# Kernel optimization log

Hardware: AMD Instinct MI355X
Metric: run time of the kernel (lower is better)

## Reference

```python
import jax, jax.numpy as jnp
import numpy as np

N, D, DEG, DEPTH, H = 50000, 300, 6, 3, 4
E = N * DEG
DK = D // H


def setup_inputs() -> dict:
    key = jax.random.key(0)
    ks = jax.random.split(key, 14)
    # circulant molecular-like graph: node i <-> i+k (k=1,2,3), edges emitted in
    # reverse pairs (2t, 2t+1) as required by reverse_edge()
    u = np.arange(N)
    src_l, dst_l = [], []
    for k in (1, 2, 3):
        v = (u + k) % N
        src_l.append(np.stack([u, v], 1).reshape(-1))
        dst_l.append(np.stack([v, u], 1).reshape(-1))
    src = np.concatenate(src_l).astype(np.int32)
    dst = np.concatenate(dst_l).astype(np.int32)
    # incoming-edge ids per node (every node has exactly DEG in-edges)
    order = np.argsort(dst, kind='stable')
    nbr_eids = order.reshape(N, DEG).astype(np.int32)
    nbr_mask = np.ones((N, DEG), dtype=bool)
    sd = 1.0 / np.sqrt(D)
    p = lambda i, shape: jax.random.normal(ks[i], shape, jnp.float32) * sd
    return {
        'f': jax.random.normal(ks[0], (N, D), jnp.float32),
        'x': jax.random.normal(ks[1], (E, D), jnp.float32),
        'Wq': p(2, (D, D)), 'bq': jnp.zeros((D,), jnp.float32),
        'Wk': p(3, (D, D)), 'bk': jnp.zeros((D,), jnp.float32),
        'Wv': p(4, (D, D)), 'bv': jnp.zeros((D,), jnp.float32),
        'Wo': p(5, (D, D)), 'bo': jnp.zeros((D,), jnp.float32),
        'W_mp': p(6, (DEPTH - 1, D, D)), 'b_mp': jnp.zeros((DEPTH - 1, D), jnp.float32),
        'W_last': p(7, (3 * D, D)), 'b_last': jnp.zeros((D,), jnp.float32),
        'src': jnp.asarray(src), 'dst': jnp.asarray(dst),
        'nbr_eids': jnp.asarray(nbr_eids), 'nbr_mask': jnp.asarray(nbr_mask),
    }


def reference(f, x, Wq, bq, Wk, bk, Wv, bv, Wo, bo, W_mp, b_mp, W_last, b_last,
              src, dst, nbr_eids, nbr_mask):
    n = f.shape[0]
    e = x.shape[0]
    rev = jnp.arange(e) ^ 1                     # reverse-pair permutation
    has_in = nbr_mask.any(axis=-1)              # [N]
    scale = 1.0 / jnp.sqrt(jnp.float32(DK))
    h = x                                       # edge state 'h' init from 'x'
    f_h = f                                     # node state 'f_h' init from 'f'
    for i in range(DEPTH - 1):
        # ragged mailbox of incoming edge states, padded to DEG
        m = jnp.where(nbr_mask[..., None], h[nbr_eids], 0.0)        # [N,DEG,D]
        q = (f_h @ Wq + bq).reshape(n, H, DK)                        # query = node feat
        k = (m @ Wk + bk).reshape(n, DEG, H, DK)                     # key   = mailbox
        v = ((m + f_h[:, None, :]) @ Wv + bv).reshape(n, DEG, H, DK) # value = mailbox + feat
        scores = jnp.einsum('nhk,ndhk->nhd', q, k) * scale          # [N,H,DEG]
        scores = jnp.where(nbr_mask[:, None, :], scores, -1e9)
        attn = jax.nn.softmax(scores, axis=-1)
        out = jnp.einsum('nhd,ndhk->nhk', attn, v).reshape(n, D) @ Wo + bo
        f_h = jnp.where(has_in[:, None], out, f_h)
        # edge update: m = f_h[src] - rev_h; h = relu(x + Linear_i(m))
        m_e = f_h[src] - h[rev]
        h = jax.nn.relu(x + m_e @ W_mp[i] + b_mp[i])
    # GEANet is undefined in the provided source -> identity pass-through
    mail = jax.ops.segment_sum(h, dst, num_segments=n)              # sum of in-edge states
    f_new = jnp.concatenate([mail, f_h, f], axis=-1) @ W_last + b_last
    f_final = jnp.where(has_in[:, None], f_new, f_h)
    return f_final, h
```

## Files before the change

kernel.cpp:

```cpp
#include <hip/hip_runtime.h>
#include <hip/hip_bf16.h>

typedef unsigned long long ull;
typedef unsigned int u32;
typedef unsigned short u16;
typedef __hip_bfloat16 bf16;
typedef __attribute__((ext_vector_type(8))) short v8s;
typedef __attribute__((ext_vector_type(4))) float v4f;
typedef __attribute__((ext_vector_type(2))) ull v2u;

#define NN 50000
#define DD 300
#define PD 320
#define EE (NN*6)

__device__ __forceinline__ u16 f2bf(float f) {
    u32 u = __float_as_uint(f);
    u32 r = u + 0x7FFFu + ((u >> 16) & 1u);
    return (u16)(r >> 16);
}
__device__ __forceinline__ float bf2f(u16 b) { return __uint_as_float(((u32)b) << 16); }

__device__ __forceinline__ ull sub4bf(ull a, ull b) {
    ull r = 0;
    #pragma unroll
    for (int i = 0; i < 4; ++i) {
        float fa = bf2f((u16)(a >> (16 * i)));
        float fb = bf2f((u16)(b >> (16 * i)));
        r |= ((ull)f2bf(fa - fb)) << (16 * i);
    }
    return r;
}

enum { A_DIR = 0, A_MPG = 1, A_CAT = 2 };
enum { E_BIAS = 0, E_RELUX = 1 };
enum { O_F32 = 1, O_BF16 = 2, O_BOTH = 3 };

template<int AMODE, int EPI, int OUTM, int NW, int NSEG>
__global__ __launch_bounds__(NW*64)
void gemm_mfma(const bf16* __restrict__ A0, const bf16* __restrict__ A1,
               const bf16* __restrict__ A2, const int* __restrict__ srcidx,
               const bf16* __restrict__ BT,
               const float* __restrict__ bias0, const float* __restrict__ bias1,
               const bf16* __restrict__ xepi,
               float* __restrict__ Cf, bf16* __restrict__ Cb0, bf16* __restrict__ Cb1,
               int M)
{
    __shared__ __align__(16) char Als[64 * 640];
    const int tid = threadIdx.x;
    const int wave = tid >> 6, lane = tid & 63;
    const int l15 = lane & 15, l4 = lane >> 4;
    const int wv = (NW == 8) ? (wave & 3) : wave;
    const int half = (NW == 8) ? (wave >> 2) : 0;
    const int rowBase = blockIdx.x * 64;
    const int T = NW * 64;

    v4f acc[4][5];
    const v4f vzero = {0.f, 0.f, 0.f, 0.f};
    #pragma unroll
    for (int mt = 0; mt < 4; ++mt)
        #pragma unroll
        for (int nt = 0; nt < 5; ++nt) acc[mt][nt] = vzero;

    for (int seg = 0; seg < NSEG; ++seg) {
        const bf16* As = (seg == 0) ? A0 : (seg == 1 ? A1 : A2);
        if (seg) __syncthreads();
        #pragma unroll
        for (int s = 0; s < 2560 / T; ++s) {
            int c = tid + T * s;
            int r = c / 40, ch = c - r * 40;
            int grow = rowBase + r;
            int gc = (grow < M) ? grow : 0;
            v2u v;
            if (AMODE == A_MPG) {
                int s0 = srcidx[gc];
                v2u a = *(const v2u*)(A0 + (long)s0 * PD + ch * 8);
                v2u b = *(const v2u*)(A1 + (long)(gc ^ 1) * PD + ch * 8);
                v[0] = sub4bf(a[0], b[0]);
                v[1] = sub4bf(a[1], b[1]);
            } else {
                v = *(const v2u*)(As + (long)gc * PD + ch * 8);
            }
            *(v2u*)(Als + ((c * 16) ^ ((r & 7) << 4))) = v;
        }
        __syncthreads();

        const bf16* BTs = BT + (long)seg * 320 * PD;
        #pragma unroll
        for (int ks = 0; ks < 10; ++ks) {
            v8s af[4];
            #pragma unroll
            for (int mt = 0; mt < 4; ++mt) {
                int rowL = mt * 16 + l15;
                af[mt] = *(const v8s*)(Als +
                    ((rowL * 640 + ks * 64 + l4 * 16) ^ ((rowL & 7) << 4)));
            }
            #pragma unroll
            for (int nt = 0; nt < 5; ++nt) {
                int col = wave * 80 + nt * 16 + l15;
                v8s bfr = *(const v8s*)(BTs + (long)col * PD + ks * 32 + l4 * 8);
                #pragma unroll
                for (int mt = 0; mt < 4; ++mt)
                    acc[mt][nt] = __builtin_amdgcn_mfma_f32_16x16x32_bf16(
                        af[mt], bfr, acc[mt][nt], 0, 0, 0);
            }
        }
        if (seg + 1 < NSEG) __syncthreads();
    }

    const int NOUT = (NW == 8) ? 2 : 1;
    #pragma unroll
    for (int oh = 0; oh < NOUT; ++oh) {
        __syncthreads();
        if (half == oh) {
            const float* bias = oh ? bias1 : bias0;
            #pragma unroll
            for (int nt = 0; nt < 5; ++nt) {
                int col = wv * 80 + nt * 16 + l15;
                float bvv = (bias && col < DD) ? bias[col] : 0.f;
                #pragma unroll
                for (int mt = 0; mt < 4; ++mt) {
                    #pragma unroll
                    for (int r = 0; r < 4; ++r) {
                        int rowL = mt * 16 + l4 * 4 + r;
                        int grow = rowBase + rowL;
                        float v = acc[mt][nt][r] + bvv;
                        if (EPI == E_RELUX) {
                            v += bf2f(((const u16*)xepi)[(long)grow * PD + col]);
                            v = fmaxf(v, 0.f);
                        }
                        if (col >= DD) v = 0.f;
                        if ((OUTM & O_F32) && grow < M && col < DD)
                            Cf[(long)grow * DD + col] = v;
                        if (OUTM & O_BF16) {
                            int addr = (rowL * 640 + col * 2) ^ (((rowL >> 2) & 7) << 4);
                            *(u16*)(Als + addr) = f2bf(v);
                        }
                    }
                }
            }
        }
        if (OUTM & O_BF16) {
            __syncthreads();
            bf16* Cb = oh ? Cb1 : Cb0;
            #pragma unroll
            for (int s = 0; s < 2560 / T; ++s) {
                int c = tid + T * s;
                int r = c / 40;
                int grow = rowBase + r;
                if (grow < M)
                    *(v2u*)(Cb + (long)grow * PD + (c - r * 40) * 8) =
                        *(const v2u*)(Als + ((c * 16) ^ (((r >> 2) & 7) << 4)));
            }
        }
    }
}

__global__ __launch_bounds__(256)
void attn_k(const bf16* __restrict__ Q, const bf16* __restrict__ FV,
            const bf16* __restrict__ Kk, const bf16* __restrict__ HV,
            const int* __restrict__ nbr, bf16* __restrict__ out)
{
    int wave = threadIdx.x >> 6, lane = threadIdx.x & 63;
    int n = blockIdx.x * 4 + wave;
    if (n >= NN) return;
    int eid[6];
    #pragma unroll
    for (int d = 0; d < 6; ++d) eid[d] = nbr[n * 6 + d];

    bool act = lane < 40;
    int cl = act ? lane : 0;
    long qo = (long)n * PD + cl * 8;
    v2u qv = *(const v2u*)(Q + qo);
    v2u fvv = *(const v2u*)(FV + qo);
    float qf[8], fvf[8];
    int hx[8];
    #pragma unroll
    for (int i = 0; i < 8; ++i) {
        u16 qr = (u16)(qv[i >> 2] >> ((i & 3) * 16));
        u16 fr = (u16)(fvv[i >> 2] >> ((i & 3) * 16));
        qf[i] = act ? bf2f(qr) : 0.f;
        fvf[i] = act ? bf2f(fr) : 0.f;
        int h = (cl * 8 + i) / 75;
        hx[i] = h > 3 ? 3 : h;
    }

    float s0[6], s1[6], s2[6], s3[6];
    #pragma unroll
    for (int d = 0; d < 6; ++d) {
        v2u kv = *(const v2u*)(Kk + (long)eid[d] * PD + cl * 8);
        float p0 = 0, p1 = 0, p2 = 0, p3 = 0;
        #pragma unroll
        for (int i = 0; i < 8; ++i) {
            float kf = bf2f((u16)(kv[i >> 2] >> ((i & 3) * 16)));
            float pr = qf[i] * kf;
            p0 += (hx[i] == 0) ? pr : 0.f;
            p1 += (hx[i] == 1) ? pr : 0.f;
            p2 += (hx[i] == 2) ? pr : 0.f;
            p3 += (hx[i] == 3) ? pr : 0.f;
        }
        #pragma unroll
        for (int off = 32; off; off >>= 1) {
            p0 += __shfl_xor(p0, off);
            p1 += __shfl_xor(p1, off);
            p2 += __shfl_xor(p2, off);
            p3 += __shfl_xor(p3, off);
        }
        s0[d] = p0; s1[d] = p1; s2[d] = p2; s3[d] = p3;
    }

    const float scale = 0.1154700538379252f;
    float at0[6], at1[6], at2[6], at3[6];
    {
        float m0 = -1e30f, m1 = -1e30f, m2 = -1e30f, m3 = -1e30f;
        #pragma unroll
        for (int d = 0; d < 6; ++d) {
            s0[d] *= scale; s1[d] *= scale; s2[d] *= scale; s3[d] *= scale;
            m0 = fmaxf(m0, s0[d]); m1 = fmaxf(m1, s1[d]);
            m2 = fmaxf(m2, s2[d]); m3 = fmaxf(m3, s3[d]);
        }
        float t0 = 0, t1 = 0, t2 = 0, t3 = 0;
        #pragma unroll
        for (int d = 0; d < 6; ++d) {
            at0[d] = expf(s0[d] - m0); t0 += at0[d];
            at1[d] = expf(s1[d] - m1); t1 += at1[d];
            at2[d] = expf(s2[d] - m2); t2 += at2[d];
            at3[d] = expf(s3[d] - m3); t3 += at3[d];
        }
        t0 = 1.f / t0; t1 = 1.f / t1; t2 = 1.f / t2; t3 = 1.f / t3;
        #pragma unroll
        for (int d = 0; d < 6; ++d) {
            at0[d] *= t0; at1[d] *= t1; at2[d] *= t2; at3[d] *= t3;
        }
    }

    float o[8];
    #pragma unroll
    for (int i = 0; i < 8; ++i) o[i] = fvf[i];
    #pragma unroll
    for (int d = 0; d < 6; ++d) {
        v2u hv = *(const v2u*)(HV + (long)eid[d] * PD + cl * 8);
        #pragma unroll
        for (int i = 0; i < 8; ++i) {
            float a = at0[d];
            a = (hx[i] == 1) ? at1[d] : a;
            a = (hx[i] == 2) ? at2[d] : a;
            a = (hx[i] == 3) ? at3[d] : a;
            o[i] += a * bf2f((u16)(hv[i >> 2] >> ((i & 3) * 16)));
        }
    }
    if (act) {
        v2u r;
        r[0] = (ull)f2bf(o[0]) | ((ull)f2bf(o[1]) << 16) |
               ((ull)f2bf(o[2]) << 32) | ((ull)f2bf(o[3]) << 48);
        r[1] = (ull)f2bf(o[4]) | ((ull)f2bf(o[5]) << 16) |
               ((ull)f2bf(o[6]) << 32) | ((ull)f2bf(o[7]) << 48);
        *(v2u*)(out + qo) = r;
    }
}

__global__ __launch_bounds__(256)
void mail_k(const bf16* __restrict__ h, const int* __restrict__ nbr,
            bf16* __restrict__ mail)
{
    int idx = blockIdx.x * 256 + threadIdx.x;
    if (idx >= NN * 40) return;
    int n = idx / 40, ch = idx - n * 40;
    const int* e = nbr + n * 6;
    float s[8] = {0, 0, 0, 0, 0, 0, 0, 0};
    #pragma unroll
    for (int d = 0; d < 6; ++d) {
        v2u v = *(const v2u*)(h + (long)e[d] * PD + ch * 8);
        #pragma unroll
        for (int i = 0; i < 8; ++i)
            s[i] += bf2f((u16)(v[i >> 2] >> ((i & 3) * 16)));
    }
    v2u r;
    r[0] = (ull)f2bf(s[0]) | ((ull)f2bf(s[1]) << 16) |
           ((ull)f2bf(s[2]) << 32) | ((ull)f2bf(s[3]) << 48);
    r[1] = (ull)f2bf(s[4]) | ((ull)f2bf(s[5]) << 16) |
           ((ull)f2bf(s[6]) << 32) | ((ull)f2bf(s[7]) << 48);
    *(v2u*)(mail + (long)n * PD + ch * 8) = r;
}

__global__ __launch_bounds__(256)
void conv_k(const float* __restrict__ in, bf16* __restrict__ out, int rows)
{
    long idx = (long)blockIdx.x * 256 + threadIdx.x;
    if (idx >= (long)rows * 40) return;
    int r = (int)(idx / 40), ch = (int)(idx - (long)r * 40);
    int c4 = ch * 2;
    float4 a = {0, 0, 0, 0}, b = {0, 0, 0, 0};
    if (c4 < 75)     a = *(const float4*)(in + (long)r * DD + c4 * 4);
    if (c4 + 1 < 75) b = *(const float4*)(in + (long)r * DD + c4 * 4 + 4);
    v2u v;
    v[0] = (ull)f2bf(a.x) | ((ull)f2bf(a.y) << 16) |
           ((ull)f2bf(a.z) << 32) | ((ull)f2bf(a.w) << 48);
    v[1] = (ull)f2bf(b.x) | ((ull)f2bf(b.y) << 16) |
           ((ull)f2bf(b.z) << 32) | ((ull)f2bf(b.w) << 48);
    *(v2u*)(out + (long)r * PD + ch * 8) = v;
}

__global__ __launch_bounds__(256)
void tw_k(const float* __restrict__ W, bf16* __restrict__ BT)
{
    int idx = blockIdx.x * 256 + threadIdx.x;
    if (idx >= 320 * 320) return;
    int nn = idx / 320, kk = idx - nn * 320;
    u16 v = 0;
    if (nn < DD && kk < DD) v = f2bf(W[kk * DD + nn]);
    ((u16*)BT)[idx] = v;
}

extern "C" void kernel_launch(void* const* d_in, const int* in_sizes, int n_in,
                              void* d_out, int out_size, void* d_ws, size_t ws_size,
                              hipStream_t stream)
{
    const float* f     = (const float*)d_in[0];
    const float* x     = (const float*)d_in[1];
    const float* Wq    = (const float*)d_in[2];
    const float* bq    = (const float*)d_in[3];
    const float* Wk    = (const float*)d_in[4];
    const float* bk    = (const float*)d_in[5];
    const float* Wv    = (const float*)d_in[6];
    const float* bv    = (const float*)d_in[7];
    const float* Wo    = (const float*)d_in[8];
    const float* bo    = (const float*)d_in[9];
    const float* Wmp   = (const float*)d_in[10];
    const float* bmp   = (const float*)d_in[11];
    const float* Wlast = (const float*)d_in[12];
    const float* blast = (const float*)d_in[13];
    const int*   src   = (const int*)d_in[14];
    const int*   nbr   = (const int*)d_in[16];

    float* out     = (float*)d_out;
    float* f_final = out;
    float* h_final = out + (long)NN * DD;

    char* ws = (char*)d_ws;
    bf16* xb  = (bf16*)(ws);
    bf16* h1b = (bf16*)(ws + 192000000LL);
    bf16* Kkb = (bf16*)(ws + 384000000LL);
    bf16* HVb = (bf16*)(ws + 576000000LL);
    bf16* fb  = (bf16*)(ws + 768000000LL);
    bf16* Qb  = (bf16*)(ws + 800000000LL);
    bf16* FVb = (bf16*)(ws + 832000000LL);
    bf16* FHb = (bf16*)(ws + 864000000LL);
    bf16* BT0 = (bf16*)(ws + 896000000LL);
    bf16* AOb = Qb;
    bf16* MLb = Qb;
    auto btp = [&](int i) { return BT0 + (long)i * 320 * 320; };

    dim3 blk(256), blk8(512);
    const int gE = (EE + 63) / 64;
    const int gN = (NN + 63) / 64;

    conv_k<<<(int)(((long)EE * 40 + 255) / 256), blk, 0, stream>>>(x, xb, EE);
    conv_k<<<(int)(((long)NN * 40 + 255) / 256), blk, 0, stream>>>(f, fb, NN);
    tw_k<<<400, blk, 0, stream>>>(Wq, btp(0));
    tw_k<<<400, blk, 0, stream>>>(Wv, btp(1));
    tw_k<<<400, blk, 0, stream>>>(Wk, btp(2));
    tw_k<<<400, blk, 0, stream>>>(Wv, btp(3));
    tw_k<<<400, blk, 0, stream>>>(Wo, btp(4));
    tw_k<<<400, blk, 0, stream>>>(Wmp, btp(5));
    tw_k<<<400, blk, 0, stream>>>(Wmp + 90000, btp(6));
    tw_k<<<400, blk, 0, stream>>>(Wlast, btp(7));
    tw_k<<<400, blk, 0, stream>>>(Wlast + 90000, btp(8));
    tw_k<<<400, blk, 0, stream>>>(Wlast + 180000, btp(9));

    for (int it = 0; it < 2; ++it) {
        const bf16* hb  = it ? h1b : xb;
        const bf16* fhb = it ? FHb : fb;
        gemm_mfma<A_DIR, E_BIAS, O_BF16, 8, 1><<<gE, blk8, 0, stream>>>(
            hb, nullptr, nullptr, nullptr, btp(2), bk, bv, nullptr,
            nullptr, Kkb, HVb, EE);
        gemm_mfma<A_DIR, E_BIAS, O_BF16, 8, 1><<<gN, blk8, 0, stream>>>(
            fhb, nullptr, nullptr, nullptr, btp(0), bq, nullptr, nullptr,
            nullptr, Qb, FVb, NN);
        attn_k<<<(NN + 3) / 4, blk, 0, stream>>>(Qb, FVb, Kkb, HVb, nbr, AOb);
        gemm_mfma<A_DIR, E_BIAS, O_BF16, 4, 1><<<gN, blk, 0, stream>>>(
            AOb, nullptr, nullptr, nullptr, btp(4), bo, nullptr, nullptr,
            nullptr, FHb, nullptr, NN);
        if (it == 0) {
            gemm_mfma<A_MPG, E_RELUX, O_BF16, 4, 1><<<gE, blk, 0, stream>>>(
                FHb, hb, nullptr, src, btp(5), bmp, nullptr, xb,
                nullptr, h1b, nullptr, EE);
        } else {
            gemm_mfma<A_MPG, E_RELUX, O_BOTH, 4, 1><<<gE, blk, 0, stream>>>(
                FHb, hb, nullptr, src, btp(6), bmp + DD, nullptr, xb,
                h_final, HVb, nullptr, EE);
        }
    }

    mail_k<<<(NN * 40 + 255) / 256, blk, 0, stream>>>(HVb, nbr, MLb);
    gemm_mfma<A_CAT, E_BIAS, O_F32, 4, 3><<<gN, blk, 0, stream>>>(
        MLb, FHb, fb, nullptr, btp(7), blast, nullptr, nullptr,
        f_final, nullptr, nullptr, NN);
}
```

Measured before the change: 2.438 ms.

## Fold Wq·Wkᵀ and Wv·Wo per head to drop edge-sized K/V GEMMs

Reassociates the attention maths so keys and values are never projected per edge. Per-head query-key matrices (Wq_h·Wk_hᵀ) and value-output matrices (Wv_h·Wo_h) are precomputed once. Scores then become dot products of node-side G_h against the raw incoming edge states, and attention-weighted sums of raw edge states feed a five-segment node GEMM. This removes the large E×D K/V GEMM from each iteration, at the cost of more node-side GEMM work, bf16-rounded composed weights, and a GEMM epilogue that now rounds to bf16 before the residual add and fp32 output.

```diff
diff --git a/kernel.cpp b/kernel.cpp
--- a/kernel.cpp
+++ b/kernel.cpp
@@ -39,8 +39,9 @@
 template<int AMODE, int EPI, int OUTM, int NW, int NSEG>
 __global__ __launch_bounds__(NW*64)
 void gemm_mfma(const bf16* __restrict__ A0, const bf16* __restrict__ A1,
-               const bf16* __restrict__ A2, const int* __restrict__ srcidx,
-               const bf16* __restrict__ BT,
+               const bf16* __restrict__ A2, const bf16* __restrict__ A3,
+               const bf16* __restrict__ A4,
+               const int* __restrict__ srcidx, const bf16* __restrict__ BT,
                const float* __restrict__ bias0, const float* __restrict__ bias1,
                const bf16* __restrict__ xepi,
                float* __restrict__ Cf, bf16* __restrict__ Cb0, bf16* __restrict__ Cb1,
@@ -63,7 +64,8 @@
         for (int nt = 0; nt < 5; ++nt) acc[mt][nt] = vzero;
 
     for (int seg = 0; seg < NSEG; ++seg) {
-        const bf16* As = (seg == 0) ? A0 : (seg == 1 ? A1 : A2);
+        const bf16* As = (seg == 0) ? A0 : (seg == 1 ? A1 : (seg == 2 ? A2 :
+                         (seg == 3 ? A3 : A4)));
         if (seg) __syncthreads();
         #pragma unroll
         for (int s = 0; s < 2560 / T; ++s) {
@@ -117,49 +119,75 @@
             #pragma unroll
             for (int nt = 0; nt < 5; ++nt) {
                 int col = wv * 80 + nt * 16 + l15;
-                float bvv = (bias && col < DD) ? bias[col] : 0.f;
+                float bvv = bias ? bias[col] : 0.f;
                 #pragma unroll
                 for (int mt = 0; mt < 4; ++mt) {
                     #pragma unroll
                     for (int r = 0; r < 4; ++r) {
                         int rowL = mt * 16 + l4 * 4 + r;
-                        int grow = rowBase + rowL;
-                        float v = acc[mt][nt][r] + bvv;
-                        if (EPI == E_RELUX) {
-                            v += bf2f(((const u16*)xepi)[(long)grow * PD + col]);
-                            v = fmaxf(v, 0.f);
+                        *(u16*)(Als + ((rowL * 640 + col * 2) ^ (((rowL >> 2) & 7) << 4)))
+                            = f2bf(acc[mt][nt][r] + bvv);
+                    }
+                }
+            }
+        }
+        __syncthreads();
+        {
+            bf16* Cb = oh ? Cb1 : Cb0;
+            #pragma unroll
+            for (int s = 0; s < 2560 / T; ++s) {
+                int c = tid + T * s;
+                int r = c / 40, ch = c - r * 40;
+                int grow = rowBase + r;
+                if (grow >= M) continue;
+                v2u val = *(const v2u*)(Als + ((c * 16) ^ (((r >> 2) & 7) << 4)));
+                if (EPI == E_RELUX) {
+                    v2u xv = *(const v2u*)(xepi + (long)grow * PD + ch * 8);
+                    #pragma unroll
+                    for (int w = 0; w < 2; ++w) {
+                        ull rr = 0;
+                        #pragma unroll
+                        for (int i = 0; i < 4; ++i) {
+                            float fv = bf2f((u16)(val[w] >> (16 * i))) +
+                                       bf2f((u16)(xv[w] >> (16 * i)));
+                            fv = fmaxf(fv, 0.f);
+                            rr |= ((ull)f2bf(fv)) << (16 * i);
                         }
-                        if (col >= DD) v = 0.f;
-                        if ((OUTM & O_F32) && grow < M && col < DD)
-                            Cf[(long)grow * DD + col] = v;
-                        if (OUTM & O_BF16) {
-                            int addr = (rowL * 640 + col * 2) ^ (((rowL >> 2) & 7) << 4);
-                            *(u16*)(Als + addr) = f2bf(v);
+                        val[w] = rr;
+                    }
+                }
+                if (OUTM & O_BF16)
+                    *(v2u*)(Cb + (long)grow * PD + ch * 8) = val;
+                if (OUTM & O_F32) {
+                    int col0 = ch * 8;
+                    if (col0 < DD) {
+                        float4 lo;
+                        lo.x = bf2f((u16)(val[0]));
+                        lo.y = bf2f((u16)(val[0] >> 16));
+                        lo.z = bf2f((u16)(val[0] >> 32));
+                        lo.w = bf2f((u16)(val[0] >> 48));
+                        *(float4*)(Cf + (long)grow * DD + col0) = lo;
+                        if (col0 + 4 < DD) {
+                            float4 hi;
+                            hi.x = bf2f((u16)(val[1]));
+                            hi.y = bf2f((u16)(val[1] >> 16));
+                            hi.z = bf2f((u16)(val[1] >> 32));
+                            hi.w = bf2f((u16)(val[1] >> 48));
+                            *(float4*)(Cf + (long)grow * DD + col0 + 4) = hi;
                         }
                     }
                 }
             }
         }
-        if (OUTM & O_BF16) {
-            __syncthreads();
-            bf16* Cb = oh ? Cb1 : Cb0;
-            #pragma unroll
-            for (int s = 0; s < 2560 / T; ++s) {
-                int c = tid + T * s;
-                int r = c / 40;
-                int grow = rowBase + r;
-                if (grow < M)
-                    *(v2u*)(Cb + (long)grow * PD + (c - r * 40) * 8) =
-                        *(const v2u*)(Als + ((c * 16) ^ (((r >> 2) & 7) << 4)));
-            }
-        }
-    }
-}
-
-__global__ __launch_bounds__(256)
-void attn_k(const bf16* __restrict__ Q, const bf16* __restrict__ FV,
-            const bf16* __restrict__ Kk, const bf16* __restrict__ HV,
-            const int* __restrict__ nbr, bf16* __restrict__ out)
+    }
+}
+
+__global__ __launch_bounds__(256)
+void scoreU_k(const bf16* __restrict__ G0, const bf16* __restrict__ G1,
+              const bf16* __restrict__ G2, const bf16* __restrict__ G3,
+              const bf16* __restrict__ h, const int* __restrict__ nbr,
+              bf16* __restrict__ U0, bf16* __restrict__ U1,
+              bf16* __restrict__ U2, bf16* __restrict__ U3)
 {
     int wave = threadIdx.x >> 6, lane = threadIdx.x & 63;
     int n = blockIdx.x * 4 + wave;
@@ -170,34 +198,33 @@
 
     bool act = lane < 40;
     int cl = act ? lane : 0;
-    long qo = (long)n * PD + cl * 8;
-    v2u qv = *(const v2u*)(Q + qo);
-    v2u fvv = *(const v2u*)(FV + qo);
-    float qf[8], fvf[8];
-    int hx[8];
-    #pragma unroll
-    for (int i = 0; i < 8; ++i) {
-        u16 qr = (u16)(qv[i >> 2] >> ((i & 3) * 16));
-        u16 fr = (u16)(fvv[i >> 2] >> ((i & 3) * 16));
-        qf[i] = act ? bf2f(qr) : 0.f;
-        fvf[i] = act ? bf2f(fr) : 0.f;
-        int h = (cl * 8 + i) / 75;
-        hx[i] = h > 3 ? 3 : h;
-    }
+    long go = (long)n * PD + cl * 8;
+
+    float g[4][8];
+    #pragma unroll
+    for (int hh = 0; hh < 4; ++hh) {
+        const bf16* Gp = (hh == 0) ? G0 : (hh == 1) ? G1 : (hh == 2) ? G2 : G3;
+        v2u gv = *(const v2u*)(Gp + go);
+        #pragma unroll
+        for (int i = 0; i < 8; ++i)
+            g[hh][i] = act ? bf2f((u16)(gv[i >> 2] >> ((i & 3) * 16))) : 0.f;
+    }
+    v2u hp[6];
+    #pragma unroll
+    for (int d = 0; d < 6; ++d)
+        hp[d] = *(const v2u*)(h + (long)eid[d] * PD + cl * 8);
 
     float s0[6], s1[6], s2[6], s3[6];
     #pragma unroll
     for (int d = 0; d < 6; ++d) {
-        v2u kv = *(const v2u*)(Kk + (long)eid[d] * PD + cl * 8);
         float p0 = 0, p1 = 0, p2 = 0, p3 = 0;
         #pragma unroll
         for (int i = 0; i < 8; ++i) {
-            float kf = bf2f((u16)(kv[i >> 2] >> ((i & 3) * 16)));
-            float pr = qf[i] * kf;
-            p0 += (hx[i] == 0) ? pr : 0.f;
-            p1 += (hx[i] == 1) ? pr : 0.f;
-            p2 += (hx[i] == 2) ? pr : 0.f;
-            p3 += (hx[i] == 3) ? pr : 0.f;
+            float hf = bf2f((u16)(hp[d][i >> 2] >> ((i & 3) * 16)));
+            p0 += g[0][i] * hf;
+            p1 += g[1][i] * hf;
+            p2 += g[2][i] * hf;
+            p3 += g[3][i] * hf;
         }
         #pragma unroll
         for (int off = 32; off; off >>= 1) {
@@ -210,7 +237,7 @@
     }
 
     const float scale = 0.1154700538379252f;
-    float at0[6], at1[6], at2[6], at3[6];
+    float at[4][6];
     {
         float m0 = -1e30f, m1 = -1e30f, m2 = -1e30f, m3 = -1e30f;
         #pragma unroll
@@ -222,40 +249,45 @@
         float t0 = 0, t1 = 0, t2 = 0, t3 = 0;
         #pragma unroll
         for (int d = 0; d < 6; ++d) {
-            at0[d] = expf(s0[d] - m0); t0 += at0[d];
-            at1[d] = expf(s1[d] - m1); t1 += at1[d];
-            at2[d] = expf(s2[d] - m2); t2 += at2[d];
-            at3[d] = expf(s3[d] - m3); t3 += at3[d];
+            at[0][d] = expf(s0[d] - m0); t0 += at[0][d];
+            at[1][d] = expf(s1[d] - m1); t1 += at[1][d];
+            at[2][d] = expf(s2[d] - m2); t2 += at[2][d];
+            at[3][d] = expf(s3[d] - m3); t3 += at[3][d];
         }
         t0 = 1.f / t0; t1 = 1.f / t1; t2 = 1.f / t2; t3 = 1.f / t3;
         #pragma unroll
         for (int d = 0; d < 6; ++d) {
-            at0[d] *= t0; at1[d] *= t1; at2[d] *= t2; at3[d] *= t3;
-        }
-    }
-
-    float o[8];
-    #pragma unroll
-    for (int i = 0; i < 8; ++i) o[i] = fvf[i];
+            at[0][d] *= t0; at[1][d] *= t1; at[2][d] *= t2; at[3][d] *= t3;
+        }
+    }
+
+    float u[4][8];
+    #pragma unroll
+    for (int hh = 0; hh < 4; ++hh)
+        #pragma unroll
+        for (int i = 0; i < 8; ++i) u[hh][i] = 0.f;
     #pragma unroll
     for (int d = 0; d < 6; ++d) {
-        v2u hv = *(const v2u*)(HV + (long)eid[d] * PD + cl * 8);
         #pragma unroll
         for (int i = 0; i < 8; ++i) {
-            float a = at0[d];
-            a = (hx[i] == 1) ? at1[d] : a;
-            a = (hx[i] == 2) ? at2[d] : a;
-            a = (hx[i] == 3) ? at3[d] : a;
-            o[i] += a * bf2f((u16)(hv[i >> 2] >> ((i & 3) * 16)));
+            float hf = bf2f((u16)(hp[d][i >> 2] >> ((i & 3) * 16)));
+            u[0][i] += at[0][d] * hf;
+            u[1][i] += at[1][d] * hf;
+            u[2][i] += at[2][d] * hf;
+            u[3][i] += at[3][d] * hf;
         }
     }
     if (act) {
-        v2u r;
-        r[0] = (ull)f2bf(o[0]) | ((ull)f2bf(o[1]) << 16) |
-               ((ull)f2bf(o[2]) << 32) | ((ull)f2bf(o[3]) << 48);
-        r[1] = (ull)f2bf(o[4]) | ((ull)f2bf(o[5]) << 16) |
-               ((ull)f2bf(o[6]) << 32) | ((ull)f2bf(o[7]) << 48);
-        *(v2u*)(out + qo) = r;
+        #pragma unroll
+        for (int hh = 0; hh < 4; ++hh) {
+            bf16* Up = (hh == 0) ? U0 : (hh == 1) ? U1 : (hh == 2) ? U2 : U3;
+            v2u r;
+            r[0] = (ull)f2bf(u[hh][0]) | ((ull)f2bf(u[hh][1]) << 16) |
+                   ((ull)f2bf(u[hh][2]) << 32) | ((ull)f2bf(u[hh][3]) << 48);
+            r[1] = (ull)f2bf(u[hh][4]) | ((ull)f2bf(u[hh][5]) << 16) |
+                   ((ull)f2bf(u[hh][6]) << 32) | ((ull)f2bf(u[hh][7]) << 48);
+            *(v2u*)(Up + go) = r;
+        }
     }
 }
 
@@ -312,6 +344,62 @@
     ((u16*)BT)[idx] = v;
 }
 
+__global__ __launch_bounds__(256)
+void wqk_k(const float* __restrict__ Wq, const float* __restrict__ Wk,
+           bf16* __restrict__ slab, int hbase)
+{
+    int idx = blockIdx.x * 256 + threadIdx.x;
+    if (idx >= 640 * 320) return;
+    int c = idx / 320, k = idx - c * 320;
+    int hh = hbase + (c >= 320 ? 1 : 0);
+    int ci = (c >= 320) ? (c - 320) : c;
+    float v = 0.f;
+    if (ci < DD && k < DD) {
+        int jb = hh * 75;
+        for (int j = 0; j < 75; ++j)
+            v += Wq[k * DD + jb + j] * Wk[ci * DD + jb + j];
+    }
+    ((u16*)slab)[idx] = f2bf(v);
+}
+
+__global__ __launch_bounds__(256)
+void wcomp_k(const float* __restrict__ Wv, const float* __restrict__ Wo,
+             bf16* __restrict__ slab)
+{
+    int idx = blockIdx.x * 256 + threadIdx.x;
+    if (idx >= 5 * 320 * 320) return;
+    int s = idx / 102400, rem = idx - s * 102400;
+    int c = rem / 320, k = rem - c * 320;
+    float v = 0.f;
+    if (c < DD && k < DD) {
+        int jb = (s < 4) ? s * 75 : 0;
+        int jn = (s < 4) ? 75 : 300;
+        for (int j = 0; j < jn; ++j)
+            v += Wv[k * DD + jb + j] * Wo[(jb + j) * DD + c];
+    }
+    ((u16*)slab)[idx] = f2bf(v);
+}
+
+__global__ void bias_k(const float* __restrict__ Wk, const float* __restrict__ Wo,
+                       const float* __restrict__ bq, const float* __restrict__ bv,
+                       const float* __restrict__ bo, const float* __restrict__ bmp,
+                       const float* __restrict__ blast, float* __restrict__ outb)
+{
+    int a = blockIdx.x, i = threadIdx.x;
+    float v = 0.f;
+    if (i < DD) {
+        if (a < 4) {
+            for (int j = 0; j < 75; ++j) v += bq[a * 75 + j] * Wk[i * DD + a * 75 + j];
+        } else if (a == 4) {
+            for (int j = 0; j < DD; ++j) v += bv[j] * Wo[j * DD + i];
+            v += bo[i];
+        } else if (a == 5) v = bmp[i];
+        else if (a == 6) v = bmp[DD + i];
+        else v = blast[i];
+    }
+    outb[a * 320 + i] = v;
+}
+
 extern "C" void kernel_launch(void* const* d_in, const int* in_sizes, int n_in,
                               void* d_out, int out_size, void* d_ws, size_t ws_size,
                               hipStream_t stream)
@@ -321,9 +409,8 @@
     const float* Wq    = (const float*)d_in[2];
     const float* bq    = (const float*)d_in[3];
     const float* Wk    = (const float*)d_in[4];
-    const float* bk    = (const float*)d_in[5];
+    const float* bv    = (const float*)d_in[7];
     const float* Wv    = (const float*)d_in[6];
-    const float* bv    = (const float*)d_in[7];
     const float* Wo    = (const float*)d_in[8];
     const float* bo    = (const float*)d_in[9];
     const float* Wmp   = (const float*)d_in[10];
@@ -340,16 +427,28 @@
     char* ws = (char*)d_ws;
     bf16* xb  = (bf16*)(ws);
     bf16* h1b = (bf16*)(ws + 192000000LL);
-    bf16* Kkb = (bf16*)(ws + 384000000LL);
-    bf16* HVb = (bf16*)(ws + 576000000LL);
-    bf16* fb  = (bf16*)(ws + 768000000LL);
-    bf16* Qb  = (bf16*)(ws + 800000000LL);
-    bf16* FVb = (bf16*)(ws + 832000000LL);
-    bf16* FHb = (bf16*)(ws + 864000000LL);
-    bf16* BT0 = (bf16*)(ws + 896000000LL);
-    bf16* AOb = Qb;
-    bf16* MLb = Qb;
-    auto btp = [&](int i) { return BT0 + (long)i * 320 * 320; };
+    bf16* h2b = (bf16*)(ws + 384000000LL);
+    bf16* fb  = (bf16*)(ws + 576000000LL);
+    bf16* G0  = (bf16*)(ws + 608000000LL);
+    bf16* G1  = (bf16*)(ws + 640000000LL);
+    bf16* G2  = (bf16*)(ws + 672000000LL);
+    bf16* G3  = (bf16*)(ws + 704000000LL);
+    bf16* FHb = (bf16*)(ws + 736000000LL);
+    bf16* WT  = (bf16*)(ws + 768000000LL);
+    float* BIAS = (float*)(ws + 772000000LL);
+    auto slot = [&](int i) { return WT + (long)i * 320 * 320; };
+    bf16* qk01 = slot(0);
+    bf16* qk23 = slot(2);
+    bf16* fh5  = slot(4);
+    bf16* mp0  = slot(9);
+    bf16* mp1  = slot(10);
+    bf16* lst  = slot(11);
+    float* g0p = BIAS;          float* g1p = BIAS + 320;
+    float* g2p = BIAS + 640;    float* g3p = BIAS + 960;
+    float* b2p = BIAS + 1280;
+    float* bm0p = BIAS + 1600;  float* bm1p = BIAS + 1920;
+    float* blp = BIAS + 2240;
+    bf16* MLb = G0;
 
     dim3 blk(256), blk8(512);
     const int gE = (EE + 63) / 64;
@@ -357,43 +456,43 @@
 
     conv_k<<<(int)(((long)EE * 40 + 255) / 256), blk, 0, stream>>>(x, xb, EE);
     conv_k<<<(int)(((long)NN * 40 + 255) / 256), blk, 0, stream>>>(f, fb, NN);
-    tw_k<<<400, blk, 0, stream>>>(Wq, btp(0));
-    tw_k<<<400, blk, 0, stream>>>(Wv, btp(1));
-    tw_k<<<400, blk, 0, stream>>>(Wk, btp(2));
-    tw_k<<<400, blk, 0, stream>>>(Wv, btp(3));
-    tw_k<<<400, blk, 0, stream>>>(Wo, btp(4));
-    tw_k<<<400, blk, 0, stream>>>(Wmp, btp(5));
-    tw_k<<<400, blk, 0, stream>>>(Wmp + 90000, btp(6));
-    tw_k<<<400, blk, 0, stream>>>(Wlast, btp(7));
-    tw_k<<<400, blk, 0, stream>>>(Wlast + 90000, btp(8));
-    tw_k<<<400, blk, 0, stream>>>(Wlast + 180000, btp(9));
+    wqk_k<<<800, blk, 0, stream>>>(Wq, Wk, qk01, 0);
+    wqk_k<<<800, blk, 0, stream>>>(Wq, Wk, qk23, 2);
+    wcomp_k<<<2000, blk, 0, stream>>>(Wv, Wo, fh5);
+    tw_k<<<400, blk, 0, stream>>>(Wmp, mp0);
+    tw_k<<<400, blk, 0, stream>>>(Wmp + 90000, mp1);
+    tw_k<<<400, blk, 0, stream>>>(Wlast, lst);
+    tw_k<<<400, blk, 0, stream>>>(Wlast + 90000, slot(12));
+    tw_k<<<400, blk, 0, stream>>>(Wlast + 180000, slot(13));
+    bias_k<<<8, 320, 0, stream>>>(Wk, Wo, bq, bv, bo, bmp, blast, BIAS);
 
     for (int it = 0; it < 2; ++it) {
         const bf16* hb  = it ? h1b : xb;
         const bf16* fhb = it ? FHb : fb;
-        gemm_mfma<A_DIR, E_BIAS, O_BF16, 8, 1><<<gE, blk8, 0, stream>>>(
-            hb, nullptr, nullptr, nullptr, btp(2), bk, bv, nullptr,
-            nullptr, Kkb, HVb, EE);
         gemm_mfma<A_DIR, E_BIAS, O_BF16, 8, 1><<<gN, blk8, 0, stream>>>(
-            fhb, nullptr, nullptr, nullptr, btp(0), bq, nullptr, nullptr,
-            nullptr, Qb, FVb, NN);
-        attn_k<<<(NN + 3) / 4, blk, 0, stream>>>(Qb, FVb, Kkb, HVb, nbr, AOb);
-        gemm_mfma<A_DIR, E_BIAS, O_BF16, 4, 1><<<gN, blk, 0, stream>>>(
-            AOb, nullptr, nullptr, nullptr, btp(4), bo, nullptr, nullptr,
+            fhb, nullptr, nullptr, nullptr, nullptr, nullptr, qk01,
+            g0p, g1p, nullptr, nullptr, G0, G1, NN);
+        gemm_mfma<A_DIR, E_BIAS, O_BF16, 8, 1><<<gN, blk8, 0, stream>>>(
+            fhb, nullptr, nullptr, nullptr, nullptr, nullptr, qk23,
+            g2p, g3p, nullptr, nullptr, G2, G3, NN);
+        scoreU_k<<<(NN + 3) / 4, blk, 0, stream>>>(G0, G1, G2, G3, hb, nbr,
+                                                   G0, G1, G2, G3);
+        gemm_mfma<A_CAT, E_BIAS, O_BF16, 4, 5><<<gN, blk, 0, stream>>>(
+            G0, G1, G2, G3, fhb, nullptr, fh5, b2p, nullptr, nullptr,
             nullptr, FHb, nullptr, NN);
         if (it == 0) {
             gemm_mfma<A_MPG, E_RELUX, O_BF16, 4, 1><<<gE, blk, 0, stream>>>(
-                FHb, hb, nullptr, src, btp(5), bmp, nullptr, xb,
-                nullptr, h1b, nullptr, EE);
+                FHb, hb, nullptr, nullptr, nullptr, src, mp0, bm0p, nullptr,
+                xb, nullptr, h1b, nullptr, EE);
         } else {
             gemm_mfma<A_MPG, E_RELUX, O_BOTH, 4, 1><<<gE, blk, 0, stream>>>(
-                FHb, hb, nullptr, src, btp(6), bmp + DD, nullptr, xb,
-                h_final, HVb, nullptr, EE);
-        }
-    }
-
-    mail_k<<<(NN * 40 + 255) / 256, blk, 0, stream>>>(HVb, nbr, MLb);
+                FHb, hb, nullptr, nullptr, nullptr, src, mp1, bm1p, nullptr,
+                xb, h_final, h2b, nullptr, EE);
+        }
+    }
+
+    mail_k<<<(NN * 40 + 255) / 256, blk, 0, stream>>>(h2b, nbr, MLb);
     gemm_mfma<A_CAT, E_BIAS, O_F32, 4, 3><<<gN, blk, 0, stream>>>(
-        MLb, FHb, fb, nullptr, btp(7), blast, nullptr, nullptr,
+        MLb, FHb, fb, nullptr, nullptr, nullptr, lst, blp, nullptr, nullptr,
         f_final, nullptr, nullptr, NN);
 }
```

Measured after the change: 2.311 ms. 1.05x faster.
